# Kernel tuning notes

Measured on AMD Instinct MI355X. Metric: run time of the kernel, lower is better.

The kernel has to match this reference:

```python
import jax, jax.numpy as jnp
import numpy as np

NUM_HEADS = 8
DIM = 256
HEAD_DIM = DIM // NUM_HEADS  # 32
CPB_HIDDEN = 512
FFN_HIDDEN = 1024


def _relative_position_cpb(query_size, key_size, pretrain_size):
    # TransNeXt-style continuous position bias table + index (query==key grid here)
    qh, qw = query_size
    kh, kw = key_size
    ph, pw = pretrain_size
    aqh = np.arange(qh, dtype=np.float64)
    akh = np.arange(kh, dtype=np.float64)
    aqw = np.arange(qw, dtype=np.float64)
    akw = np.arange(kw, dtype=np.float64)
    kH, kW = np.meshgrid(akh, akw, indexing='ij')
    qH, qW = np.meshgrid(aqh, aqw, indexing='ij')
    rel_h = (qH.reshape(-1)[:, None] - kH.reshape(-1)[None, :]) / (ph - 1) * 8.0
    rel_w = (qW.reshape(-1)[:, None] - kW.reshape(-1)[None, :]) / (pw - 1) * 8.0
    rel = np.stack([rel_h, rel_w], axis=-1).reshape(-1, 2)
    table, idx = np.unique(rel, return_inverse=True, axis=0)
    table = np.sign(table) * np.log2(np.abs(table) + 1.0) / np.log2(8.0)
    return idx.astype(np.int32).reshape(-1), table.astype(np.float32)


def setup_inputs() -> dict:
    key = jax.random.key(0)
    ks = jax.random.split(key, 16)
    B, C, H, W = 8, 256, 128, 128
    q = jax.random.normal(ks[0], (B, C, H, W), dtype=jnp.float32)
    kv = jax.random.normal(ks[1], (B, C, H, W), dtype=jnp.float32)
    rel_idx_np, rel_table_np = _relative_position_cpb((32, 32), (32, 32), (32, 32))
    s = 0.02
    inp = {
        'q': q,
        'kv': kv,
        'rel_pos_index': jnp.asarray(rel_idx_np),
        'rel_coords_table': jnp.asarray(rel_table_np),
        'Wq': jax.random.normal(ks[2], (DIM, DIM), jnp.float32) * s,
        'bq': jnp.zeros((DIM,), jnp.float32),
        'Wkv': jax.random.normal(ks[3], (DIM, 2 * DIM), jnp.float32) * s,
        'bkv': jnp.zeros((2 * DIM,), jnp.float32),
        'Wo': jax.random.normal(ks[4], (DIM, DIM), jnp.float32) * s,
        'bo': jnp.zeros((DIM,), jnp.float32),
        'cpb_w1': jax.random.normal(ks[5], (2, CPB_HIDDEN), jnp.float32) * s,
        'cpb_b1': jnp.zeros((CPB_HIDDEN,), jnp.float32),
        'cpb_w2': jax.random.normal(ks[6], (CPB_HIDDEN, NUM_HEADS), jnp.float32) * s,
        'cpb_b2': jnp.zeros((NUM_HEADS,), jnp.float32),
        'ffn_w1': jax.random.normal(ks[7], (DIM, FFN_HIDDEN), jnp.float32) * s,
        'ffn_b1': jnp.zeros((FFN_HIDDEN,), jnp.float32),
        'ffn_w2': jax.random.normal(ks[8], (FFN_HIDDEN, DIM), jnp.float32) * s,
        'ffn_b2': jnp.zeros((DIM,), jnp.float32),
        'ln_g': jnp.ones((DIM,), jnp.float32),
        'ln_b': jnp.zeros((DIM,), jnp.float32),
    }
    return inp


def _resize_bilinear(x, size):
    # matches torch F.interpolate(mode='bilinear', align_corners=False)
    return jax.image.resize(x, (x.shape[0], x.shape[1], size[0], size[1]),
                            method='linear', antialias=False)


def _layernorm(x, g, b, eps=1e-5):
    mu = jnp.mean(x, axis=-1, keepdims=True)
    var = jnp.mean(jnp.square(x - mu), axis=-1, keepdims=True)
    return (x - mu) * jax.lax.rsqrt(var + eps) * g + b


def _fpn_forward(q, kv, rel_pos_index, rel_coords_table, Wq, bq, Wkv, bkv, Wo, bo,
                 cpb_w1, cpb_b1, cpb_w2, cpb_b2, ffn_w1, ffn_b1, ffn_w2, ffn_b2, ln_g, ln_b):
    x = q
    B, C, H, W = q.shape
    pH = H // 4
    pW = H // 4  # note: original code uses h for both, matching square inputs
    N = pH * pW

    qd = jax.nn.relu(_resize_bilinear(q, (pH, pW)))   # [B,C,pH,pW] (dropout p=0)
    kvd = jax.nn.relu(_resize_bilinear(kv, (pH, pW)))
    qt = qd.reshape(B, C, N).transpose(0, 2, 1)   # [B,N,C]
    kvt = kvd.reshape(B, C, N).transpose(0, 2, 1)  # [B,N,C]

    # --- BVAM: cross-attention with continuous relative position bias ---
    qh = (qt @ Wq + bq).reshape(B, N, NUM_HEADS, HEAD_DIM).transpose(0, 2, 1, 3)  # [B,h,N,d]
    kvp = (kvt @ Wkv + bkv).reshape(B, N, 2, NUM_HEADS, HEAD_DIM).transpose(2, 0, 3, 1, 4)
    k, v = kvp[0], kvp[1]  # [B,h,N,d]

    cpb = jax.nn.relu(rel_coords_table @ cpb_w1 + cpb_b1) @ cpb_w2 + cpb_b2  # [L,h]
    bias = cpb[rel_pos_index].reshape(N, N, NUM_HEADS).transpose(2, 0, 1)    # [h,N,N]

    scale = 1.0 / jnp.sqrt(jnp.float32(HEAD_DIM))
    logits = jnp.einsum('bhnd,bhmd->bhnm', qh, k) * scale + bias[None]
    attn = jax.nn.softmax(logits, axis=-1)
    out = jnp.einsum('bhnm,bhmd->bhnd', attn, v)
    out = out.transpose(0, 2, 1, 3).reshape(B, N, C) @ Wo + bo  # [B,N,C]

    # --- FFN (post-norm, gelu) ---
    ff = jax.nn.gelu(out @ ffn_w1 + ffn_b1, approximate=False) @ ffn_w2 + ffn_b2
    y = _layernorm(out + ff, ln_g, ln_b)  # [B,N,C]

    # back to spatial, upsample, residual
    y = y.transpose(0, 2, 1).reshape(B, C, pH, pW)
    y = jax.nn.relu(_resize_bilinear(y, (H, W)))
    return x + y


def reference(q, kv, rel_pos_index, rel_coords_table, Wq, bq, Wkv, bkv, Wo, bo,
              cpb_w1, cpb_b1, cpb_w2, cpb_b2, ffn_w1, ffn_b1, ffn_w2, ffn_b2, ln_g, ln_b):
    return _fpn_forward(q, kv, rel_pos_index, rel_coords_table, Wq, bq, Wkv, bkv, Wo, bo,
                        cpb_w1, cpb_b1, cpb_w2, cpb_b2, ffn_w1, ffn_b1, ffn_w2, ffn_b2, ln_g, ln_b)
```

## Files before the change

### kernel.cpp

```cpp
#include <hip/hip_runtime.h>
#include <hip/hip_bf16.h>
#include <hip/hip_fp16.h>

typedef __hip_bfloat16 bf16;
typedef __attribute__((ext_vector_type(8))) __bf16 bf16x8;
typedef __attribute__((ext_vector_type(4))) __bf16 bf16x4;
typedef __attribute__((ext_vector_type(4))) float f32x4;
typedef __attribute__((ext_vector_type(4))) float f4;

__device__ __forceinline__ void gload_lds16(const bf16* g, bf16* l)
{
    __builtin_amdgcn_global_load_lds((const __attribute__((address_space(1))) void*)g,
                                     (__attribute__((address_space(3))) void*)l, 16, 0, 0);
}

__global__ __launch_bounds__(256) void prep_kernel(
    const float* __restrict__ tab, const float* __restrict__ w1, const float* __restrict__ b1,
    const float* __restrict__ w2, const float* __restrict__ b2, float* __restrict__ cpbout, int L, int ncpb,
    const float* __restrict__ Wq, const float* __restrict__ Wkv, const float* __restrict__ Wo,
    const float* __restrict__ fw1, const float* __restrict__ fw2,
    bf16* __restrict__ WqT, bf16* __restrict__ WkvT, bf16* __restrict__ WoT,
    bf16* __restrict__ W1T, bf16* __restrict__ W2T,
    const float* __restrict__ qsrc, const float* __restrict__ kvsrc,
    bf16* __restrict__ qdst, bf16* __restrict__ kvdst)
{
    __shared__ float o[32][33];
    const int t = threadIdx.x;
    int bid = blockIdx.x;
    if (bid < ncpb) {
        int l = bid * 32 + (t >> 3);
        int js = t & 7;
        bool valid = l < L;
        float t0 = valid ? tab[2 * l] : 0.f, t1 = valid ? tab[2 * l + 1] : 0.f;
        float acc[8];
#pragma unroll
        for (int hh = 0; hh < 8; ++hh) acc[hh] = 0.f;
        for (int j = js; j < 512; j += 8) {
            float hv = fmaxf(t0 * w1[j] + t1 * w1[512 + j] + b1[j], 0.f);
            f4 w2a = *(const f4*)&w2[j * 8];
            f4 w2b = *(const f4*)&w2[j * 8 + 4];
#pragma unroll
            for (int hh = 0; hh < 4; ++hh) { acc[hh] += hv * w2a[hh]; acc[4 + hh] += hv * w2b[hh]; }
        }
#pragma unroll
        for (int d = 1; d < 8; d <<= 1)
#pragma unroll
            for (int hh = 0; hh < 8; ++hh) acc[hh] += __shfl_xor(acc[hh], d);
        if (js == 0 && valid)
#pragma unroll
            for (int hh = 0; hh < 8; ++hh) cpbout[(size_t)hh * L + l] = acc[hh] + b2[hh];
        return;
    }
    bid -= ncpb;
    if (bid < 768) {
        const float* W; bf16* WT; int K, N, base;
        if (bid < 64)        { W = Wq;  WT = WqT;  K = 256;  N = 256;  base = 0; }
        else if (bid < 192)  { W = Wkv; WT = WkvT; K = 256;  N = 512;  base = 64; }
        else if (bid < 256)  { W = Wo;  WT = WoT;  K = 256;  N = 256;  base = 192; }
        else if (bid < 512)  { W = fw1; WT = W1T;  K = 256;  N = 1024; base = 256; }
        else                 { W = fw2; WT = W2T;  K = 1024; N = 256;  base = 512; }
        int lid = bid - base;
        int tn = N >> 5;
        int k0 = (lid / tn) << 5, n0 = (lid % tn) << 5;
        {
            int r = t >> 3, cc = (t & 7) * 4;
            *(f4*)&o[r][cc] = *(const f4*)&W[(size_t)(k0 + r) * N + n0 + cc];
        }
        __syncthreads();
        {
            int n = t >> 3, kk = (t & 7) * 4;
            bf16 tmp[4];
#pragma unroll
            for (int i = 0; i < 4; ++i) tmp[i] = (bf16)o[kk + i][n];
            *(bf16x4*)&WT[(size_t)(n0 + n) * K + k0 + kk] = *(const bf16x4*)tmp;
        }
        return;
    }
    bid -= 768;
    {
        const float* src = bid < 2048 ? qsrc : kvsrc;
        bf16* dst = bid < 2048 ? qdst : kvdst;
        int bb2 = bid & 2047;
        int cc = bb2 & 7, i = (bb2 >> 3) & 31, b = bb2 >> 8;
#pragma unroll
        for (int p = 0; p < 4; ++p) {
            int id = p * 256 + t;
            int c = id >> 5, j = id & 31;
            const float* r = src + ((size_t)(b * 256 + cc * 32 + c) * 128 + 4 * i + 1) * 128 + 4 * j;
            float4 r1 = *(const float4*)r;
            float4 r2 = *(const float4*)(r + 128);
            o[c][j] = 0.25f * (r1.y + r1.z + r2.y + r2.z);
        }
        __syncthreads();
        {
            int j = t >> 3, c4 = (t & 7) * 4;
            bf16 tmp[4];
#pragma unroll
            for (int k = 0; k < 4; ++k) tmp[k] = (bf16)fmaxf(o[c4 + k][j], 0.f);
            *(bf16x4*)&dst[(size_t)(b * 1024 + i * 32 + j) * 256 + cc * 32 + c4] = *(const bf16x4*)tmp;
        }
    }
}

template<int BM, int BN>
__device__ __forceinline__ void gemm_core(
    const bf16* __restrict__ A, const bf16* __restrict__ BT, int K,
    int m0, int n0, bf16* As, bf16* Bs, f32x4 (&acc)[BM / 32][BN / 32])
{
    constexpr int MI = BM / 32, NJ = BN / 32;
    const int tid = threadIdx.x;
    const int lane = tid & 63, wid = tid >> 6;
    const int lo = lane & 15, hi = lane >> 4;
    const int wr = wid >> 1, wc = wid & 1;
#pragma unroll
    for (int i = 0; i < MI; ++i)
#pragma unroll
        for (int j = 0; j < NJ; ++j) acc[i][j] = f32x4{0.f, 0.f, 0.f, 0.f};

    for (int k0 = 0; k0 < K; k0 += 64) {
        __syncthreads();
#pragma unroll
        for (int p = 0; p < BM / 32; ++p) {
            int f = p * 256 + wid * 64 + lane;
            int row = f >> 3, cs = f & 7;
            gload_lds16(&A[(size_t)(m0 + row) * K + k0 + ((cs ^ (row & 7)) * 8)],
                        As + (size_t)(p * 256 + wid * 64) * 8);
        }
#pragma unroll
        for (int p = 0; p < BN / 32; ++p) {
            int f = p * 256 + wid * 64 + lane;
            int row = f >> 3, cs = f & 7;
            gload_lds16(&BT[(size_t)(n0 + row) * K + k0 + ((cs ^ (row & 7)) * 8)],
                        Bs + (size_t)(p * 256 + wid * 64) * 8);
        }
        __syncthreads();
        bf16x8 af[2][MI], bfr[2][NJ];
#pragma unroll
        for (int kk = 0; kk < 2; ++kk) {
#pragma unroll
            for (int i = 0; i < MI; ++i) {
                int row = wr * (BM / 2) + i * 16 + lo;
                af[kk][i] = *(const bf16x8*)&As[row * 64 + (((kk * 4 + hi) ^ (lo & 7)) * 8)];
            }
#pragma unroll
            for (int j = 0; j < NJ; ++j) {
                int row = wc * (BN / 2) + j * 16 + lo;
                bfr[kk][j] = *(const bf16x8*)&Bs[row * 64 + (((kk * 4 + hi) ^ (lo & 7)) * 8)];
            }
        }
#pragma unroll
        for (int kk = 0; kk < 2; ++kk)
#pragma unroll
            for (int i = 0; i < MI; ++i)
#pragma unroll
                for (int j = 0; j < NJ; ++j)
                    acc[i][j] = __builtin_amdgcn_mfma_f32_16x16x32_bf16(af[kk][i], bfr[kk][j], acc[i][j], 0, 0, 0);
    }
}

template<int BM, int BN>
__global__ __launch_bounds__(256) void gemm_bt(
    const bf16* __restrict__ A, const bf16* __restrict__ BT,
    const float* __restrict__ bias, bf16* __restrict__ Cb, float* __restrict__ Cf,
    const bf16* __restrict__ resid, int M, int N, int K, int act)
{
    constexpr int MI = BM / 32, NJ = BN / 32;
    __shared__ __align__(16) bf16 As[BM * 64];
    __shared__ __align__(16) bf16 Bs[BN * 64];
    const int tid = threadIdx.x;
    const int lane = tid & 63, wid = tid >> 6;
    const int lo = lane & 15, hi = lane >> 4;
    const int m0 = blockIdx.x * BM, n0 = blockIdx.y * BN;
    const int wr = wid >> 1, wc = wid & 1;
    f32x4 acc[MI][NJ];
    gemm_core<BM, BN>(A, BT, K, m0, n0, As, Bs, acc);
#pragma unroll
    for (int i = 0; i < MI; ++i)
#pragma unroll
        for (int j = 0; j < NJ; ++j) {
            int col = n0 + wc * (BN / 2) + j * 16 + lo;
            float bv = bias[col];
#pragma unroll
            for (int r = 0; r < 4; ++r) {
                int row = m0 + wr * (BM / 2) + i * 16 + hi * 4 + r;
                float v = acc[i][j][r] + bv;
                if (act == 1) v = 0.5f * v * (1.f + erff(v * 0.70710678118654752f));
                if (resid) v += (float)resid[(size_t)row * N + col];
                if (Cb) Cb[(size_t)row * N + col] = (bf16)v;
                else    Cf[(size_t)row * N + col] = v;
            }
        }
}

__global__ __launch_bounds__(256) void gemm_qkv(
    const bf16* __restrict__ qt, const bf16* __restrict__ WqT, const float* __restrict__ bq,
    bf16* __restrict__ qhb,
    const bf16* __restrict__ kvt, const bf16* __restrict__ WkvT, const float* __restrict__ bkv,
    bf16* __restrict__ kvpb, bf16* __restrict__ vT,
    const int* __restrict__ ridx, const float* __restrict__ cpbh,
    bf16* __restrict__ biasF, int L)
{
    __shared__ __align__(16) bf16 As[64 * 64];
    __shared__ __align__(16) bf16 Bs[64 * 64];
    const int tid = threadIdx.x;
    const int lane = tid & 63, wid = tid >> 6;
    const int lo = lane & 15, hi = lane >> 4;
    const int by = blockIdx.y;
    if (by >= 12) {
        __shared__ int rix[32][32];
        int id = (by - 12) * 128 + blockIdx.x;
        int qtb = id >> 5, mt = id & 31;
        {
            int q = tid >> 3, m4 = (tid & 7) * 4;
            *(int4*)&rix[q][m4] = *(const int4*)&ridx[(size_t)(qtb * 32 + q) * 1024 + mt * 32 + m4];
        }
        __syncthreads();
        const int qj = (tid >> 6) & 1, hg = tid >> 7;
        int lidx[8];
#pragma unroll
        for (int j = 0; j < 8; ++j) {
            int kf = j >> 2, r = j & 3;
            lidx[j] = rix[qj * 16 + lo][kf * 16 + hi * 4 + r];
        }
#pragma unroll
        for (int hh = 0; hh < 4; ++hh) {
            int h = hg * 4 + hh;
            const float* ct = cpbh + (size_t)h * L;
            bf16 vals[8];
#pragma unroll
            for (int j = 0; j < 8; ++j) vals[j] = (bf16)ct[lidx[j]];
            size_t off = ((((size_t)(h * 32 + qtb) * 32 + mt) * 2 + qj) * 64 + lane) * 8;
            *(bf16x8*)&biasF[off] = *(const bf16x8*)vals;
        }
        return;
    }
    const int wr = wid >> 1, wc = wid & 1;
    const bf16 *A, *BT; const float* bias; int n0;
    if (by < 4)      { A = qt;  BT = WqT;  bias = bq;  n0 = by * 64; }
    else             { A = kvt; BT = WkvT; bias = bkv; n0 = (by - 4) * 64; }
    const int m0 = blockIdx.x * 64;
    f32x4 acc[2][2];
    gemm_core<64, 64>(A, BT, 256, m0, n0, As, Bs, acc);
#pragma unroll
    for (int i = 0; i < 2; ++i)
#pragma unroll
        for (int j = 0; j < 2; ++j) {
            int col = n0 + wc * 32 + j * 16 + lo;
            float bv = bias[col];
            if (by < 4) {
#pragma unroll
                for (int r = 0; r < 4; ++r) {
                    int row = m0 + wr * 32 + i * 16 + hi * 4 + r;
                    qhb[(size_t)row * 256 + col] = (bf16)(acc[i][j][r] + bv);
                }
            } else if (by < 8) {
#pragma unroll
                for (int r = 0; r < 4; ++r) {
                    int row = m0 + wr * 32 + i * 16 + hi * 4 + r;
                    kvpb[(size_t)row * 512 + col] = (bf16)(acc[i][j][r] + bv);
                }
            } else {
                int vcol = col - 256;
                int h = vcol >> 5, d = vcol & 31;
                int b = m0 >> 10;
                int mbase = (m0 & 1023) + wr * 32 + i * 16 + hi * 4;
                bf16 tmp[4];
#pragma unroll
                for (int r = 0; r < 4; ++r) tmp[r] = (bf16)(acc[i][j][r] + bv);
                *(bf16x4*)&vT[(size_t)((b * 8 + h) * 32 + d) * 1024 + mbase] = *(const bf16x4*)tmp;
            }
        }
}

__global__ __launch_bounds__(256) void ffn2_ln_kernel(
    const bf16* __restrict__ A, const bf16* __restrict__ BT,
    const float* __restrict__ bias, const bf16* __restrict__ resid,
    const float* __restrict__ g, const float* __restrict__ bb,
    bf16* __restrict__ ysp)
{
    __shared__ __align__(16) bf16 As[16 * 64];
    __shared__ __align__(16) bf16 Bs[256 * 64];
    __shared__ float buf[16][260];
    const int tid = threadIdx.x;
    const int lane = tid & 63, wid = tid >> 6;
    const int lo = lane & 15, hi = lane >> 4;
    const int m0 = blockIdx.x * 16;
    f32x4 acc[4];
#pragma unroll
    for (int j = 0; j < 4; ++j) acc[j] = f32x4{0.f, 0.f, 0.f, 0.f};

    for (int k0 = 0; k0 < 1024; k0 += 64) {
        __syncthreads();
        if (tid < 128) {
            int row = tid >> 3, cs = tid & 7;
            gload_lds16(&A[(size_t)(m0 + row) * 1024 + k0 + ((cs ^ (row & 7)) * 8)],
                        As + (size_t)(wid * 64) * 8);
        }
#pragma unroll
        for (int p = 0; p < 8; ++p) {
            int f = p * 256 + tid, row = f >> 3, cs = f & 7;
            gload_lds16(&BT[(size_t)row * 1024 + k0 + ((cs ^ (row & 7)) * 8)],
                        Bs + (size_t)(p * 256 + wid * 64) * 8);
        }
        __syncthreads();
        bf16x8 af[2], bfr[2][4];
#pragma unroll
        for (int kk = 0; kk < 2; ++kk) {
            af[kk] = *(const bf16x8*)&As[lo * 64 + (((kk * 4 + hi) ^ (lo & 7)) * 8)];
#pragma unroll
            for (int j = 0; j < 4; ++j) {
                int row = wid * 64 + j * 16 + lo;
                bfr[kk][j] = *(const bf16x8*)&Bs[row * 64 + (((kk * 4 + hi) ^ (lo & 7)) * 8)];
            }
        }
#pragma unroll
        for (int kk = 0; kk < 2; ++kk)
#pragma unroll
            for (int j = 0; j < 4; ++j)
                acc[j] = __builtin_amdgcn_mfma_f32_16x16x32_bf16(af[kk], bfr[kk][j], acc[j], 0, 0, 0);
    }
#pragma unroll
    for (int j = 0; j < 4; ++j) {
        int col = wid * 64 + j * 16 + lo;
        float bv = bias[col];
#pragma unroll
        for (int r = 0; r < 4; ++r) {
            int lr = hi * 4 + r;
            buf[lr][col] = acc[j][r] + bv + (float)resid[(size_t)(m0 + lr) * 256 + col];
        }
    }
    __syncthreads();
#pragma unroll
    for (int rr = 0; rr < 4; ++rr) {
        int row = wid * 4 + rr;
        f4 x = *(const f4*)&buf[row][lane * 4];
        float s = x[0] + x[1] + x[2] + x[3];
#pragma unroll
        for (int d = 1; d < 64; d <<= 1) s += __shfl_xor(s, d);
        float mean = s * (1.f / 256.f);
        f4 dv = {x[0] - mean, x[1] - mean, x[2] - mean, x[3] - mean};
        float s2 = dv[0] * dv[0] + dv[1] * dv[1] + dv[2] * dv[2] + dv[3] * dv[3];
#pragma unroll
        for (int d = 1; d < 64; d <<= 1) s2 += __shfl_xor(s2, d);
        float rstd = rsqrtf(s2 * (1.f / 256.f) + 1e-5f);
        f4 o = {dv[0] * rstd, dv[1] * rstd, dv[2] * rstd, dv[3] * rstd};
        *(f4*)&buf[row][lane * 4] = o;
    }
    __syncthreads();
    float gc = g[tid], bc = bb[tid];
    int b = m0 >> 10, n0l = m0 & 1023;
    bf16* dst = &ysp[((size_t)(b * 256 + tid) << 10) + n0l];
#pragma unroll
    for (int p = 0; p < 2; ++p) {
        bf16 tmp[8];
#pragma unroll
        for (int k = 0; k < 8; ++k) tmp[k] = (bf16)(buf[p * 8 + k][tid] * gc + bc);
        *(bf16x8*)&dst[p * 8] = *(const bf16x8*)tmp;
    }
}

__global__ __launch_bounds__(256) void attn_kernel(
    const bf16* __restrict__ qh, const bf16* __restrict__ kvp, const bf16* __restrict__ vT,
    const bf16* __restrict__ biasF, bf16* __restrict__ attnout)
{
    __shared__ __align__(16) bf16 Ps[4][32 * 40];
    __shared__ __align__(16) __half accs[4][32][34];
    __shared__ float pm[4][32], pl[4][32];
    const int tid = threadIdx.x, lane = tid & 63, wid = tid >> 6;
    const int lo = lane & 15, hi = lane >> 4;
    const int qt = blockIdx.x, n0 = qt * 32;
    const int h = blockIdx.y;
    const int b = blockIdx.z;
    const float scale = 0.17677669529663687f;
    const f32x4 zero4 = {0.f, 0.f, 0.f, 0.f};

    bf16x8 qf[2];
#pragma unroll
    for (int qj = 0; qj < 2; ++qj)
        qf[qj] = *(const bf16x8*)&qh[(size_t)(b * 1024 + n0 + qj * 16 + lo) * 256 + h * 32 + hi * 8];

    f32x4 acc[2][2];
#pragma unroll
    for (int i = 0; i < 2; ++i)
#pragma unroll
        for (int j = 0; j < 2; ++j) acc[i][j] = zero4;
    float mrow[2] = {-1e30f, -1e30f}, lrow[2] = {0.f, 0.f};

    bf16* Pw = Ps[wid];

    for (int t = wid; t < 32; t += 4) {
        const int m0 = t * 32;
        bf16x8 kfr0 = *(const bf16x8*)&kvp[(size_t)(b * 1024 + m0 + lo) * 512 + h * 32 + hi * 8];
        bf16x8 kfr1 = *(const bf16x8*)&kvp[(size_t)(b * 1024 + m0 + 16 + lo) * 512 + h * 32 + hi * 8];
        bf16x8 va0 = *(const bf16x8*)&vT[(size_t)((b * 8 + h) * 32 + lo) * 1024 + m0 + hi * 8];
        bf16x8 va1 = *(const bf16x8*)&vT[(size_t)((b * 8 + h) * 32 + 16 + lo) * 1024 + m0 + hi * 8];
        size_t boff = (((size_t)(h * 32 + qt) * 32 + t) * 2 * 64 + lane) * 8;
        bf16x8 bv0 = *(const bf16x8*)&biasF[boff];
        bf16x8 bv1 = *(const bf16x8*)&biasF[boff + 512];

        f32x4 s[2][2];
        s[0][0] = __builtin_amdgcn_mfma_f32_16x16x32_bf16(kfr0, qf[0], zero4, 0, 0, 0);
        s[0][1] = __builtin_amdgcn_mfma_f32_16x16x32_bf16(kfr0, qf[1], zero4, 0, 0, 0);
        s[1][0] = __builtin_amdgcn_mfma_f32_16x16x32_bf16(kfr1, qf[0], zero4, 0, 0, 0);
        s[1][1] = __builtin_amdgcn_mfma_f32_16x16x32_bf16(kfr1, qf[1], zero4, 0, 0, 0);
#pragma unroll
        for (int kf = 0; kf < 2; ++kf)
#pragma unroll
            for (int r = 0; r < 4; ++r) {
                s[kf][0][r] = s[kf][0][r] * scale + (float)bv0[kf * 4 + r];
                s[kf][1][r] = s[kf][1][r] * scale + (float)bv1[kf * 4 + r];
            }
#pragma unroll
        for (int qj = 0; qj < 2; ++qj) {
            float mx = fmaxf(fmaxf(fmaxf(s[0][qj][0], s[0][qj][1]), fmaxf(s[0][qj][2], s[0][qj][3])),
                             fmaxf(fmaxf(s[1][qj][0], s[1][qj][1]), fmaxf(s[1][qj][2], s[1][qj][3])));
            mx = fmaxf(mx, __shfl_xor(mx, 16));
            mx = fmaxf(mx, __shfl_xor(mx, 32));
            float mnew = fmaxf(mrow[qj], mx);
            float alpha = __expf(mrow[qj] - mnew);
            float rs = 0.f;
#pragma unroll
            for (int kf = 0; kf < 2; ++kf)
#pragma unroll
                for (int r = 0; r < 4; ++r) {
                    float p = __expf(s[kf][qj][r] - mnew);
                    s[kf][qj][r] = p;
                    rs += p;
                }
            rs += __shfl_xor(rs, 16);
            rs += __shfl_xor(rs, 32);
            lrow[qj] = lrow[qj] * alpha + rs;
            mrow[qj] = mnew;
#pragma unroll
            for (int di = 0; di < 2; ++di)
#pragma unroll
                for (int r = 0; r < 4; ++r) acc[di][qj][r] *= alpha;
        }
#pragma unroll
        for (int qj = 0; qj < 2; ++qj)
#pragma unroll
            for (int kf = 0; kf < 2; ++kf)
#pragma unroll
                for (int r = 0; r < 4; ++r)
                    Pw[(qj * 16 + lo) * 40 + kf * 16 + hi * 4 + r] = (bf16)s[kf][qj][r];
        bf16x8 pb0 = *(const bf16x8*)&Pw[lo * 40 + hi * 8];
        bf16x8 pb1 = *(const bf16x8*)&Pw[(16 + lo) * 40 + hi * 8];
        acc[0][0] = __builtin_amdgcn_mfma_f32_16x16x32_bf16(va0, pb0, acc[0][0], 0, 0, 0);
        acc[0][1] = __builtin_amdgcn_mfma_f32_16x16x32_bf16(va0, pb1, acc[0][1], 0, 0, 0);
        acc[1][0] = __builtin_amdgcn_mfma_f32_16x16x32_bf16(va1, pb0, acc[1][0], 0, 0, 0);
        acc[1][1] = __builtin_amdgcn_mfma_f32_16x16x32_bf16(va1, pb1, acc[1][1], 0, 0, 0);
    }
#pragma unroll
    for (int di = 0; di < 2; ++di)
#pragma unroll
        for (int qj = 0; qj < 2; ++qj)
#pragma unroll
            for (int r = 0; r < 4; ++r)
                accs[wid][di * 16 + hi * 4 + r][qj * 16 + lo] = __float2half(acc[di][qj][r]);
    if (hi == 0) {
#pragma unroll
        for (int qj = 0; qj < 2; ++qj) {
            pm[wid][qj * 16 + lo] = mrow[qj];
            pl[wid][qj * 16 + lo] = lrow[qj];
        }
    }
    __syncthreads();
    int q = tid >> 3, d0 = (tid & 7) * 4;
    float M = fmaxf(fmaxf(pm[0][q], pm[1][q]), fmaxf(pm[2][q], pm[3][q]));
    float f0 = __expf(pm[0][q] - M), f1 = __expf(pm[1][q] - M);
    float f2 = __expf(pm[2][q] - M), f3 = __expf(pm[3][q] - M);
    float inv = 1.f / (pl[0][q] * f0 + pl[1][q] * f1 + pl[2][q] * f2 + pl[3][q] * f3);
    bf16 tmp[4];
#pragma unroll
    for (int j = 0; j < 4; ++j) {
        int d = d0 + j;
        float o = f0 * (float)accs[0][d][q] + f1 * (float)accs[1][d][q] +
                  f2 * (float)accs[2][d][q] + f3 * (float)accs[3][d][q];
        tmp[j] = (bf16)(o * inv);
    }
    *(bf16x4*)&attnout[(size_t)(b * 1024 + n0 + q) * 256 + h * 32 + d0] = *(const bf16x4*)tmp;
}

__global__ __launch_bounds__(256) void upsample_kernel(const float* __restrict__ x,
    const bf16* __restrict__ ysp, float* __restrict__ out)
{
    int idx = blockIdx.x * 256 + threadIdx.x;
    int w4 = idx & 31; int r1 = idx >> 5;
    int hh = r1 & 127; int r2 = r1 >> 7;
    int c = r2 & 255; int b = r2 >> 8;
    float chh = 0.25f * hh - 0.375f;
    float fi = floorf(chh);
    float fh = chh - fi;
    int i0 = (int)fi;
    int ia = i0 < 0 ? 0 : i0;
    int ib = (i0 + 1) > 31 ? 31 : (i0 + 1);
    const bf16* yr = ysp + ((size_t)(b * 256 + c) << 10);
    const bf16* ra = yr + ia * 32;
    const bf16* rb = yr + ib * 32;
    f4 xv = *(const f4*)&x[(size_t)idx * 4];
    f4 o;
#pragma unroll
    for (int k = 0; k < 4; ++k) {
        int ww = w4 * 4 + k;
        float cww = 0.25f * ww - 0.375f;
        float fj = floorf(cww);
        float fw = cww - fj;
        int j0 = (int)fj;
        int ja = j0 < 0 ? 0 : j0;
        int jb = (j0 + 1) > 31 ? 31 : (j0 + 1);
        float v = (1.f - fh) * ((1.f - fw) * (float)ra[ja] + fw * (float)ra[jb]) +
                  fh * ((1.f - fw) * (float)rb[ja] + fw * (float)rb[jb]);
        o[k] = xv[k] + fmaxf(v, 0.f);
    }
    *(f4*)&out[(size_t)idx * 4] = o;
}

extern "C" void kernel_launch(void* const* d_in, const int* in_sizes, int n_in,
                              void* d_out, int out_size, void* d_ws, size_t ws_size,
                              hipStream_t stream)
{
    (void)n_in; (void)out_size; (void)ws_size;
    const float* q    = (const float*)d_in[0];
    const float* kv   = (const float*)d_in[1];
    const int*   ridx = (const int*)d_in[2];
    const float* rtab = (const float*)d_in[3];
    const float* Wq   = (const float*)d_in[4];
    const float* bq   = (const float*)d_in[5];
    const float* Wkv  = (const float*)d_in[6];
    const float* bkv  = (const float*)d_in[7];
    const float* Wo   = (const float*)d_in[8];
    const float* bo   = (const float*)d_in[9];
    const float* cw1  = (const float*)d_in[10];
    const float* cb1  = (const float*)d_in[11];
    const float* cw2  = (const float*)d_in[12];
    const float* cb2  = (const float*)d_in[13];
    const float* fw1  = (const float*)d_in[14];
    const float* fb1  = (const float*)d_in[15];
    const float* fw2  = (const float*)d_in[16];
    const float* fb2  = (const float*)d_in[17];
    const float* lng  = (const float*)d_in[18];
    const float* lnb  = (const float*)d_in[19];
    const int L = in_sizes[3] / 2;
    const int ncpb = (L + 31) / 32;

    char* w = (char*)d_ws;
    auto alloc = [&](size_t bytes) { char* p = w; w += (bytes + 255) & ~(size_t)255; return p; };
    bf16* qt      = (bf16*)alloc(8192ull * 256 * 2);
    bf16* kvt     = (bf16*)alloc(8192ull * 256 * 2);
    bf16* qhb     = (bf16*)alloc(8192ull * 256 * 2);
    bf16* kvpb    = (bf16*)alloc(8192ull * 512 * 2);
    bf16* vTb     = (bf16*)alloc(8ull * 8 * 32 * 1024 * 2);
    bf16* attnb   = (bf16*)alloc(8192ull * 256 * 2);
    bf16* outb    = (bf16*)alloc(8192ull * 256 * 2);
    bf16* ffh     = (bf16*)alloc(8192ull * 1024 * 2);
    bf16* ysp     = (bf16*)alloc(8ull * 256 * 1024 * 2);
    bf16* WqT     = (bf16*)alloc(256ull * 256 * 2);
    bf16* WkvT    = (bf16*)alloc(512ull * 256 * 2);
    bf16* WoT     = (bf16*)alloc(256ull * 256 * 2);
    bf16* W1T     = (bf16*)alloc(1024ull * 256 * 2);
    bf16* W2T     = (bf16*)alloc(256ull * 1024 * 2);
    float* cpbb   = (float*)alloc((size_t)8 * L * 4);
    bf16* biasF   = ffh;

    prep_kernel<<<dim3(ncpb + 768 + 4096), 256, 0, stream>>>(
        rtab, cw1, cb1, cw2, cb2, cpbb, L, ncpb,
        Wq, Wkv, Wo, fw1, fw2, WqT, WkvT, WoT, W1T, W2T,
        q, kv, qt, kvt);
    gemm_qkv<<<dim3(128, 20), 256, 0, stream>>>(qt, WqT, bq, qhb, kvt, WkvT, bkv, kvpb, vTb,
                                                ridx, cpbb, biasF, L);
    attn_kernel<<<dim3(32, 8, 8), 256, 0, stream>>>(qhb, kvpb, vTb, biasF, attnb);
    gemm_bt<64, 64><<<dim3(128, 4), 256, 0, stream>>>(attnb, WoT, bo, outb, nullptr, nullptr, 8192, 256, 256, 0);
    gemm_bt<128, 64><<<dim3(64, 16), 256, 0, stream>>>(outb, W1T, fb1, ffh, nullptr, nullptr, 8192, 1024, 256, 1);
    ffn2_ln_kernel<<<dim3(512), 256, 0, stream>>>(ffh, W2T, fb2, outb, lng, lnb, ysp);
    upsample_kernel<<<dim3(32768), 256, 0, stream>>>(q, ysp, (float*)d_out);
}
```

Measured before the change: 189.2 us.

## Swap FFN1 grid order, raise MFMA priority in attention, simplify upsample

Three separate tweaks. The FFN1 GEMM grid is transposed so that consecutive blocks walk the N tiles of the same M row block, which is meant to improve L2 reuse of the A tile. The attention MFMA sections are wrapped in s_setprio so the matrix instructions get issue priority. The bilinear upsample drops the per-pixel floor and index arithmetic, uses the fixed 4x weights with three neighbour loads, and writes its output with nontemporal stores. The hardcoded weights assume the exact 32-to-128 scale factor.

Result: faster. 173.1 us (-8.5%).

```diff
diff --git a/kernel.cpp b/kernel.cpp
--- a/kernel.cpp
+++ b/kernel.cpp
@@ -158,7 +158,7 @@
     }
 }
 
-template<int BM, int BN>
+template<int BM, int BN, bool SWAP>
 __global__ __launch_bounds__(256) void gemm_bt(
     const bf16* __restrict__ A, const bf16* __restrict__ BT,
     const float* __restrict__ bias, bf16* __restrict__ Cb, float* __restrict__ Cf,
@@ -170,7 +170,8 @@
     const int tid = threadIdx.x;
     const int lane = tid & 63, wid = tid >> 6;
     const int lo = lane & 15, hi = lane >> 4;
-    const int m0 = blockIdx.x * BM, n0 = blockIdx.y * BN;
+    const int m0 = (SWAP ? blockIdx.y : blockIdx.x) * BM;
+    const int n0 = (SWAP ? blockIdx.x : blockIdx.y) * BN;
     const int wr = wid >> 1, wc = wid & 1;
     f32x4 acc[MI][NJ];
     gemm_core<BM, BN>(A, BT, K, m0, n0, As, Bs, acc);
@@ -399,10 +400,12 @@
         bf16x8 bv1 = *(const bf16x8*)&biasF[boff + 512];
 
         f32x4 s[2][2];
+        __builtin_amdgcn_s_setprio(1);
         s[0][0] = __builtin_amdgcn_mfma_f32_16x16x32_bf16(kfr0, qf[0], zero4, 0, 0, 0);
         s[0][1] = __builtin_amdgcn_mfma_f32_16x16x32_bf16(kfr0, qf[1], zero4, 0, 0, 0);
         s[1][0] = __builtin_amdgcn_mfma_f32_16x16x32_bf16(kfr1, qf[0], zero4, 0, 0, 0);
         s[1][1] = __builtin_amdgcn_mfma_f32_16x16x32_bf16(kfr1, qf[1], zero4, 0, 0, 0);
+        __builtin_amdgcn_s_setprio(0);
 #pragma unroll
         for (int kf = 0; kf < 2; ++kf)
 #pragma unroll
@@ -445,10 +448,12 @@
                     Pw[(qj * 16 + lo) * 40 + kf * 16 + hi * 4 + r] = (bf16)s[kf][qj][r];
         bf16x8 pb0 = *(const bf16x8*)&Pw[lo * 40 + hi * 8];
         bf16x8 pb1 = *(const bf16x8*)&Pw[(16 + lo) * 40 + hi * 8];
+        __builtin_amdgcn_s_setprio(1);
         acc[0][0] = __builtin_amdgcn_mfma_f32_16x16x32_bf16(va0, pb0, acc[0][0], 0, 0, 0);
         acc[0][1] = __builtin_amdgcn_mfma_f32_16x16x32_bf16(va0, pb1, acc[0][1], 0, 0, 0);
         acc[1][0] = __builtin_amdgcn_mfma_f32_16x16x32_bf16(va1, pb0, acc[1][0], 0, 0, 0);
         acc[1][1] = __builtin_amdgcn_mfma_f32_16x16x32_bf16(va1, pb1, acc[1][1], 0, 0, 0);
+        __builtin_amdgcn_s_setprio(0);
     }
 #pragma unroll
     for (int di = 0; di < 2; ++di)
@@ -485,34 +490,41 @@
     const bf16* __restrict__ ysp, float* __restrict__ out)
 {
     int idx = blockIdx.x * 256 + threadIdx.x;
-    int w4 = idx & 31; int r1 = idx >> 5;
+    int m = idx & 31; int r1 = idx >> 5;
     int hh = r1 & 127; int r2 = r1 >> 7;
     int c = r2 & 255; int b = r2 >> 8;
-    float chh = 0.25f * hh - 0.375f;
-    float fi = floorf(chh);
-    float fh = chh - fi;
-    int i0 = (int)fi;
+    const int rr = hh & 3, n = hh >> 2;
+    const float fh = (rr == 0) ? 0.625f : (rr == 1) ? 0.875f : (rr == 2) ? 0.125f : 0.375f;
+    int i0 = n + ((rr >= 2) ? 0 : -1);
     int ia = i0 < 0 ? 0 : i0;
     int ib = (i0 + 1) > 31 ? 31 : (i0 + 1);
     const bf16* yr = ysp + ((size_t)(b * 256 + c) << 10);
     const bf16* ra = yr + ia * 32;
     const bf16* rb = yr + ib * 32;
+    int jm1 = m > 0 ? m - 1 : 0;
+    int jp1 = m < 31 ? m + 1 : 31;
+    float am1 = (float)ra[jm1], a0 = (float)ra[m], ap1 = (float)ra[jp1];
+    float bm1 = (float)rb[jm1], b0 = (float)rb[m], bp1 = (float)rb[jp1];
+    const float gh = 1.f - fh;
     f4 xv = *(const f4*)&x[(size_t)idx * 4];
     f4 o;
-#pragma unroll
-    for (int k = 0; k < 4; ++k) {
-        int ww = w4 * 4 + k;
-        float cww = 0.25f * ww - 0.375f;
-        float fj = floorf(cww);
-        float fw = cww - fj;
-        int j0 = (int)fj;
-        int ja = j0 < 0 ? 0 : j0;
-        int jb = (j0 + 1) > 31 ? 31 : (j0 + 1);
-        float v = (1.f - fh) * ((1.f - fw) * (float)ra[ja] + fw * (float)ra[jb]) +
-                  fh * ((1.f - fw) * (float)rb[ja] + fw * (float)rb[jb]);
-        o[k] = xv[k] + fmaxf(v, 0.f);
-    }
-    *(f4*)&out[(size_t)idx * 4] = o;
+    {
+        float ta = 0.375f * am1 + 0.625f * a0, tb = 0.375f * bm1 + 0.625f * b0;
+        o[0] = xv[0] + fmaxf(gh * ta + fh * tb, 0.f);
+    }
+    {
+        float ta = 0.125f * am1 + 0.875f * a0, tb = 0.125f * bm1 + 0.875f * b0;
+        o[1] = xv[1] + fmaxf(gh * ta + fh * tb, 0.f);
+    }
+    {
+        float ta = 0.875f * a0 + 0.125f * ap1, tb = 0.875f * b0 + 0.125f * bp1;
+        o[2] = xv[2] + fmaxf(gh * ta + fh * tb, 0.f);
+    }
+    {
+        float ta = 0.625f * a0 + 0.375f * ap1, tb = 0.625f * b0 + 0.375f * bp1;
+        o[3] = xv[3] + fmaxf(gh * ta + fh * tb, 0.f);
+    }
+    __builtin_nontemporal_store(o, (f4*)&out[(size_t)idx * 4]);
 }
 
 extern "C" void kernel_launch(void* const* d_in, const int* in_sizes, int n_in,
@@ -569,8 +581,8 @@
     gemm_qkv<<<dim3(128, 20), 256, 0, stream>>>(qt, WqT, bq, qhb, kvt, WkvT, bkv, kvpb, vTb,
                                                 ridx, cpbb, biasF, L);
     attn_kernel<<<dim3(32, 8, 8), 256, 0, stream>>>(qhb, kvpb, vTb, biasF, attnb);
-    gemm_bt<64, 64><<<dim3(128, 4), 256, 0, stream>>>(attnb, WoT, bo, outb, nullptr, nullptr, 8192, 256, 256, 0);
-    gemm_bt<128, 64><<<dim3(64, 16), 256, 0, stream>>>(outb, W1T, fb1, ffh, nullptr, nullptr, 8192, 1024, 256, 1);
+    gemm_bt<64, 64, false><<<dim3(128, 4), 256, 0, stream>>>(attnb, WoT, bo, outb, nullptr, nullptr, 8192, 256, 256, 0);
+    gemm_bt<128, 64, true><<<dim3(16, 64), 256, 0, stream>>>(outb, W1T, fb1, ffh, nullptr, nullptr, 8192, 1024, 256, 1);
     ffn2_ln_kernel<<<dim3(512), 256, 0, stream>>>(ffh, W2T, fb2, outb, lng, lnb, ysp);
     upsample_kernel<<<dim3(32768), 256, 0, stream>>>(q, ysp, (float*)d_out);
 }
```
